# Performance work log

Hardware: AMD Instinct MI355X
Metric: run time of the kernel (lower is better)

The kernel has to match this reference:

```python
import jax, jax.numpy as jnp
import numpy as np

B, S, D, H = 2, 2048, 1024, 16
DH = D // H  # per-head attention dim


def setup_inputs() -> dict:
    key = jax.random.key(0)
    ks = jax.random.split(key, 11)
    scale = 0.02
    return {
        "query": jax.random.normal(ks[0], (B, S, D), jnp.float32),
        "key": jax.random.normal(ks[1], (B, S, D), jnp.float32),
        "value": jax.random.normal(ks[2], (B, S, D), jnp.float32),
        # per-head QKV projection weights, stacked over heads: [H, D, DH]
        "Wq": jax.random.normal(ks[3], (H, D, DH), jnp.float32) * scale,
        "bq": jnp.zeros((H, DH), jnp.float32),
        "Wk": jax.random.normal(ks[4], (H, D, DH), jnp.float32) * scale,
        "bk": jnp.zeros((H, DH), jnp.float32),
        "Wv": jax.random.normal(ks[5], (H, D, DH), jnp.float32) * scale,
        "bv": jnp.zeros((H, DH), jnp.float32),
        # output linear: [D, D]
        "Wo": jax.random.normal(ks[6], (D, D), jnp.float32) * scale,
        "bo": jnp.zeros((D,), jnp.float32),
        "look_ahead_mask": 1,
    }


def reference(query, key, value, Wq, bq, Wk, bk, Wv, bv, Wo, bo, look_ahead_mask):
    # batched per-head projections: [B,S,D] x [H,D,E] -> [B,H,S,E]
    q = jnp.einsum("bsd,hde->bhse", query, Wq) + bq[None, :, None, :]
    k = jnp.einsum("bsd,hde->bhse", key, Wk) + bk[None, :, None, :]
    v = jnp.einsum("bsd,hde->bhse", value, Wv) + bv[None, :, None, :]
    scores = jnp.einsum("bhqe,bhke->bhqk", q, k) / jnp.sqrt(jnp.float32(DH))
    if look_ahead_mask:
        causal = jnp.tril(jnp.ones((S, S), bool))
        scores = jnp.where(causal[None, None], scores, jnp.float32(-1e9))
    probs = jax.nn.softmax(scores, axis=-1)
    ctx = jnp.einsum("bhqk,bhke->bhqe", probs, v)  # [B,H,S,DH]
    # concat heads along last dim (head order matches ModuleList order)
    concat = ctx.transpose(0, 2, 1, 3).reshape(B, S, D)
    return concat @ Wo + bo
```

## Files before the change

kernel.cpp:

```cpp
#include <hip/hip_runtime.h>


typedef short bf16x8 __attribute__((ext_vector_type(8)));
typedef float f32x4 __attribute__((ext_vector_type(4)));

__device__ __forceinline__ unsigned short f2bf(float f){
  unsigned int u = __builtin_bit_cast(unsigned int, f);
  u = (u + 0x7fffu + ((u >> 16) & 1u)) >> 16;
  return (unsigned short)u;
}

__device__ __forceinline__ void gld_lds16(const void* src, void* dst){
  __builtin_amdgcn_global_load_lds((const __attribute__((address_space(1))) unsigned int*)src,
                                   (__attribute__((address_space(3))) unsigned int*)dst,
                                   16, 0, 0);
}

__device__ __forceinline__ void stage_lds(const char* gtile, size_t growb, char* lds,
                                          int tid, int rowb_lg2, int swz, int tilebytes){
  int w = tid >> 6;
  for (int c = 0; c < tilebytes; c += 4096){
    int o = c + tid*16;
    int row = o >> rowb_lg2;
    int colb = o & ((1 << rowb_lg2) - 1);
    if (swz) colb ^= ((row & 7) << 4);
    gld_lds16(gtile + (size_t)row*growb + colb, lds + c + w*1024);
  }
}

__global__ __launch_bounds__(256) void convert3(const float* __restrict__ a,
                                                const float* __restrict__ b,
                                                const float* __restrict__ c,
                                                unsigned short* __restrict__ outa,
                                                unsigned short* __restrict__ outb,
                                                unsigned short* __restrict__ outc){
  int i = blockIdx.x*blockDim.x + threadIdx.x;
  int seg = i >> 19, il = i & 524287;
  const float* in = seg==0 ? a : (seg==1 ? b : c);
  unsigned short* out = seg==0 ? outa : (seg==1 ? outb : outc);
  const float4* p = (const float4*)in;
  float4 x = p[2*il], y = p[2*il+1];
  uint4 o;
  o.x = (unsigned int)f2bf(x.x) | ((unsigned int)f2bf(x.y) << 16);
  o.y = (unsigned int)f2bf(x.z) | ((unsigned int)f2bf(x.w) << 16);
  o.z = (unsigned int)f2bf(y.x) | ((unsigned int)f2bf(y.y) << 16);
  o.w = (unsigned int)f2bf(y.z) | ((unsigned int)f2bf(y.w) << 16);
  ((uint4*)out)[il] = o;
}

__global__ __launch_bounds__(256) void transpose_bf16(const float* __restrict__ in,
                                                      unsigned short* __restrict__ out,
                                                      int R, int C,
                                                      size_t in_mstride, size_t out_mstride){
  __shared__ unsigned short tile[64][66];
  int t = threadIdx.x;
  int r0 = blockIdx.x*64, c0 = blockIdx.y*64;
  const float* inm = in + (size_t)blockIdx.z*in_mstride;
  unsigned short* outm = out + (size_t)blockIdx.z*out_mstride;
  int j = t & 63, i0 = (t >> 6)*16;
  #pragma unroll
  for (int ii = 0; ii < 16; ii++){
    int i = i0 + ii;
    tile[i][j] = f2bf(inm[(size_t)(r0+i)*C + c0 + j]);
  }
  __syncthreads();
  #pragma unroll
  for (int ii = 0; ii < 16; ii++){
    int i = i0 + ii;
    outm[(size_t)(c0+i)*R + r0 + j] = tile[j][i];
  }
}

__global__ __launch_bounds__(256) void transpose_v(const unsigned short* __restrict__ in,
                                                   unsigned short* __restrict__ out){
  __shared__ unsigned short tile[64][66];
  int t = threadIdx.x;
  int s0 = blockIdx.x*64;
  const unsigned short* inm = in + (size_t)blockIdx.y*131072;
  unsigned short* outm = out + (size_t)blockIdx.y*131072;
  int j = t & 63, i0 = (t >> 6)*16;
  #pragma unroll
  for (int ii = 0; ii < 16; ii++){
    int i = i0 + ii;
    tile[i][j] = inm[(size_t)(s0+i)*64 + j];
  }
  __syncthreads();
  #pragma unroll
  for (int ii = 0; ii < 16; ii++){
    int i = i0 + ii;
    outm[(size_t)i*2048 + s0 + j] = tile[j][i];
  }
}

template<int EPI>
__device__ __forceinline__ void gemm_body(const unsigned short* A, const unsigned short* BT,
                                          const float* bias, void* outp, float scale,
                                          unsigned short (*lA)[128*32], unsigned short (*lB)[128*32]){
  const int K = 1024, N = 1024;
  int tid = threadIdx.x, lane = tid & 63, w = tid >> 6;
  int bn = blockIdx.x*128, bm = blockIdx.y*128;
  int wm = (w >> 1)*64, wn = (w & 1)*64;
  int lr = lane & 15;
  int lkb = (lane >> 4)*16;
  const char* Ab = (const char*)(A + (size_t)bm*K);
  const char* Bb = (const char*)(BT + (size_t)bn*K);
  size_t grow = (size_t)K*2;
  int nk = K >> 5;

  f32x4 zf = {0.f,0.f,0.f,0.f};
  f32x4 acc[4][4];
  #pragma unroll
  for (int mi = 0; mi < 4; mi++)
    #pragma unroll
    for (int ni = 0; ni < 4; ni++) acc[mi][ni] = zf;

  stage_lds(Ab, grow, (char*)lA[0], tid, 6, 0, 8192);
  stage_lds(Bb, grow, (char*)lB[0], tid, 6, 0, 8192);
  __syncthreads();
  int cur = 0;
  for (int kt = 0; kt < nk; kt++){
    if (kt + 1 < nk){
      stage_lds(Ab + (size_t)(kt+1)*64, grow, (char*)lA[cur^1], tid, 6, 0, 8192);
      stage_lds(Bb + (size_t)(kt+1)*64, grow, (char*)lB[cur^1], tid, 6, 0, 8192);
    }
    const char* pa = (const char*)lA[cur];
    const char* pb = (const char*)lB[cur];
    bf16x8 af[4], bfr[4];
    #pragma unroll
    for (int mi = 0; mi < 4; mi++)
      af[mi] = *(const bf16x8*)(pa + (wm + mi*16 + lr)*64 + lkb);
    #pragma unroll
    for (int ni = 0; ni < 4; ni++)
      bfr[ni] = *(const bf16x8*)(pb + (wn + ni*16 + lr)*64 + lkb);
    #pragma unroll
    for (int mi = 0; mi < 4; mi++)
      #pragma unroll
      for (int ni = 0; ni < 4; ni++)
        acc[mi][ni] = __builtin_amdgcn_mfma_f32_16x16x32_bf16(af[mi], bfr[ni], acc[mi][ni], 0, 0, 0);
    __syncthreads();
    cur ^= 1;
  }

  #pragma unroll
  for (int mi = 0; mi < 4; mi++)
    #pragma unroll
    for (int ni = 0; ni < 4; ni++)
      #pragma unroll
      for (int r = 0; r < 4; r++){
        int row = bm + wm + mi*16 + (lane >> 4)*4 + r;
        int col = bn + wn + ni*16 + (lane & 15);
        float v = acc[mi][ni][r] + bias[col];
        if (EPI == 0){
          v *= scale;
          unsigned short* o = (unsigned short*)outp;
          o[(size_t)((row >> 11)*16 + (col >> 6))*131072 + (size_t)(row & 2047)*64 + (col & 63)] = f2bf(v);
        } else {
          float* o = (float*)outp;
          o[(size_t)row*N + col] = v;
        }
      }
}

__global__ __launch_bounds__(256) void gemm_qkv(const unsigned short* __restrict__ Xq,
                                                const unsigned short* __restrict__ Xk,
                                                const unsigned short* __restrict__ Xv,
                                                const unsigned short* __restrict__ WqT,
                                                const unsigned short* __restrict__ WkT,
                                                const unsigned short* __restrict__ WvT,
                                                const float* __restrict__ bq,
                                                const float* __restrict__ bk,
                                                const float* __restrict__ bv,
                                                unsigned short* __restrict__ oq,
                                                unsigned short* __restrict__ ok,
                                                unsigned short* __restrict__ ov){
  __shared__ __align__(16) unsigned short lA[2][128*32];
  __shared__ __align__(16) unsigned short lB[2][128*32];
  int z = blockIdx.z;
  const unsigned short* A  = z==0 ? Xq  : (z==1 ? Xk  : Xv);
  const unsigned short* BT = z==0 ? WqT : (z==1 ? WkT : WvT);
  const float* bias        = z==0 ? bq  : (z==1 ? bk  : bv);
  unsigned short* out      = z==0 ? oq  : (z==1 ? ok  : ov);
  float scale = z==0 ? 0.125f : 1.0f;
  gemm_body<0>(A, BT, bias, out, scale, lA, lB);
}

__global__ __launch_bounds__(256) void gemm_out(const unsigned short* __restrict__ A,
                                                const unsigned short* __restrict__ BT,
                                                const float* __restrict__ bias,
                                                float* __restrict__ outp){
  __shared__ __align__(16) unsigned short lA[2][128*32];
  __shared__ __align__(16) unsigned short lB[2][128*32];
  gemm_body<1>(A, BT, bias, outp, 1.0f, lA, lB);
}

__global__ __launch_bounds__(256) void attn_fwd2(const unsigned short* __restrict__ qh,
                                                 const unsigned short* __restrict__ kh,
                                                 const unsigned short* __restrict__ vt,
                                                 unsigned short* __restrict__ cc,
                                                 const int* __restrict__ maskp){
  __shared__ __align__(16) unsigned short Ps[4][16*64];
  int tid = threadIdx.x, lane = tid & 63, w = tid >> 6;
  int lg = lane >> 4, lr = lane & 15;
  int bid = blockIdx.x;
  int bh = bid & 31;
  int qquad = 31 - (bid >> 5);
  int causal = *maskp;
  int g = qquad*4 + w;
  int wq0 = g*16;
  const char* Q  = (const char*)(qh + (size_t)bh*131072);
  const char* K  = (const char*)(kh + (size_t)bh*131072);
  const char* VT = (const char*)(vt + (size_t)bh*131072);

  bf16x8 qf[2];
  #pragma unroll
  for (int kk = 0; kk < 2; kk++)
    qf[kk] = *(const bf16x8*)(Q + (size_t)(wq0 + lr)*128 + kk*64 + lg*16);

  f32x4 zf = {0.f,0.f,0.f,0.f};
  f32x4 oa[4];
  float mr[4], lsm[4];
  #pragma unroll
  for (int ei = 0; ei < 4; ei++) oa[ei] = zf;
  #pragma unroll
  for (int r = 0; r < 4; r++){ mr[r] = -1e30f; lsm[r] = 0.f; }

  int nt = causal ? (qquad + 1) : 32;

  for (int t = 0; t < nt; t++){
    bf16x8 kf[2][4];
    #pragma unroll
    for (int kk = 0; kk < 2; kk++)
      #pragma unroll
      for (int ni = 0; ni < 4; ni++)
        kf[kk][ni] = *(const bf16x8*)(K + (size_t)(t*64 + ni*16 + lr)*128 + kk*64 + lg*16);

    f32x4 sc[4];
    #pragma unroll
    for (int ni = 0; ni < 4; ni++) sc[ni] = zf;
    #pragma unroll
    for (int kk = 0; kk < 2; kk++)
      #pragma unroll
      for (int ni = 0; ni < 4; ni++)
        sc[ni] = __builtin_amdgcn_mfma_f32_16x16x32_bf16(qf[kk], kf[kk][ni], sc[ni], 0, 0, 0);

    if (causal && (t*64 + 63 > wq0)){
      #pragma unroll
      for (int ni = 0; ni < 4; ni++)
        #pragma unroll
        for (int r = 0; r < 4; r++){
          int qrow = wq0 + lg*4 + r;
          int kvc  = t*64 + ni*16 + lr;
          if (kvc > qrow) sc[ni][r] = -1e9f;
        }
    }

    #pragma unroll
    for (int r = 0; r < 4; r++){
      float mx = fmaxf(fmaxf(sc[0][r], sc[1][r]), fmaxf(sc[2][r], sc[3][r]));
      #pragma unroll
      for (int off = 1; off < 16; off <<= 1)
        mx = fmaxf(mx, __shfl_xor(mx, off, 64));
      float mo = mr[r];
      float mn = fmaxf(mo, mx);
      mr[r] = mn;
      float alpha = __expf(mo - mn);
      float psum = 0.f;
      #pragma unroll
      for (int ni = 0; ni < 4; ni++){
        float p = __expf(sc[ni][r] - mn);
        sc[ni][r] = p;
        psum += p;
      }
      #pragma unroll
      for (int off = 1; off < 16; off <<= 1)
        psum += __shfl_xor(psum, off, 64);
      lsm[r] = lsm[r]*alpha + psum;
      #pragma unroll
      for (int ei = 0; ei < 4; ei++) oa[ei][r] *= alpha;
    }

    #pragma unroll
    for (int ni = 0; ni < 4; ni++)
      #pragma unroll
      for (int r = 0; r < 4; r++){
        int prow = lg*4 + r;
        int pcb = (ni*16 + lr)*2;
        *(unsigned short*)((char*)Ps[w] + prow*128 + (pcb ^ ((prow & 7) << 4))) = f2bf(sc[ni][r]);
      }

    #pragma unroll
    for (int kk = 0; kk < 2; kk++){
      bf16x8 pf = *(const bf16x8*)((const char*)Ps[w] + lr*128 + ((kk*64 + lg*16) ^ ((lr & 7) << 4)));
      #pragma unroll
      for (int ei = 0; ei < 4; ei++){
        bf16x8 vf = *(const bf16x8*)(VT + (size_t)(ei*16 + lr)*4096 + t*128 + kk*64 + lg*16);
        oa[ei] = __builtin_amdgcn_mfma_f32_16x16x32_bf16(pf, vf, oa[ei], 0, 0, 0);
      }
    }
  }

  int b = bh >> 4, h = bh & 15;
  #pragma unroll
  for (int r = 0; r < 4; r++){
    float inv = 1.f / lsm[r];
    int q = wq0 + lg*4 + r;
    size_t rowbase = (size_t)(b*2048 + q)*1024 + h*64;
    #pragma unroll
    for (int ei = 0; ei < 4; ei++){
      int e = ei*16 + lr;
      cc[rowbase + e] = f2bf(oa[ei][r] * inv);
    }
  }
}

extern "C" void kernel_launch(void* const* d_in, const int* in_sizes, int n_in,
                              void* d_out, int out_size, void* d_ws, size_t ws_size,
                              hipStream_t stream){
  const float* query = (const float*)d_in[0];
  const float* key_i = (const float*)d_in[1];
  const float* value = (const float*)d_in[2];
  const float* Wq = (const float*)d_in[3];
  const float* bq = (const float*)d_in[4];
  const float* Wk = (const float*)d_in[5];
  const float* bk = (const float*)d_in[6];
  const float* Wv = (const float*)d_in[7];
  const float* bv = (const float*)d_in[8];
  const float* Wo = (const float*)d_in[9];
  const float* bo = (const float*)d_in[10];
  const int* mask = (const int*)d_in[11];

  char* ws = (char*)d_ws;
  const size_t ACT = 8388608;
  unsigned short* Xq  = (unsigned short*)(ws + 0*ACT);
  unsigned short* Xk  = (unsigned short*)(ws + 1*ACT);
  unsigned short* Xv  = (unsigned short*)(ws + 2*ACT);
  unsigned short* qh  = (unsigned short*)(ws + 3*ACT);
  unsigned short* kh  = (unsigned short*)(ws + 4*ACT);
  unsigned short* vh  = (unsigned short*)(ws + 5*ACT);
  unsigned short* cc  = (unsigned short*)(ws + 6*ACT);
  unsigned short* WqT = (unsigned short*)(ws + 7*ACT);
  unsigned short* WkT = (unsigned short*)(ws + 7*ACT + 2097152);
  unsigned short* WvT = (unsigned short*)(ws + 7*ACT + 4194304);
  unsigned short* WoT = (unsigned short*)(ws + 7*ACT + 6291456);
  unsigned short* vtr = Xq;

  convert3<<<6144, 256, 0, stream>>>(query, key_i, value, Xq, Xk, Xv);

  transpose_bf16<<<dim3(16,1,16), 256, 0, stream>>>(Wq, WqT, 1024, 64, 65536, 65536);
  transpose_bf16<<<dim3(16,1,16), 256, 0, stream>>>(Wk, WkT, 1024, 64, 65536, 65536);
  transpose_bf16<<<dim3(16,1,16), 256, 0, stream>>>(Wv, WvT, 1024, 64, 65536, 65536);
  transpose_bf16<<<dim3(16,16,1), 256, 0, stream>>>(Wo, WoT, 1024, 1024, 0, 0);

  gemm_qkv<<<dim3(8,32,3), 256, 0, stream>>>(Xq, Xk, Xv, WqT, WkT, WvT, bq, bk, bv, qh, kh, vh);

  transpose_v<<<dim3(32,32), 256, 0, stream>>>(vh, vtr);

  attn_fwd2<<<1024, 256, 0, stream>>>(qh, kh, vtr, cc, mask);

  gemm_out<<<dim3(8,32), 256, 0, stream>>>(cc, WoT, bo, (float*)d_out);
}
```

Baseline: 336.7 us.

## Pair low and high causal query tiles per block sharing K/V loads

Each attention block now handles two query tiles, p and 31-p, so every block does the same amount of causal work, and it launches half as many blocks. The K and V fragments loaded for each KV tile feed both query tiles, and the next K tile is prefetched into registers. A launch-bounds occupancy hint is added. The cost is higher register pressure from two sets of accumulators and prefetch buffers, and fewer blocks in flight.

```diff
diff --git a/kernel.cpp b/kernel.cpp
--- a/kernel.cpp
+++ b/kernel.cpp
@@ -193,122 +193,171 @@
   gemm_body<1>(A, BT, bias, outp, 1.0f, lA, lB);
 }
 
-__global__ __launch_bounds__(256) void attn_fwd2(const unsigned short* __restrict__ qh,
-                                                 const unsigned short* __restrict__ kh,
-                                                 const unsigned short* __restrict__ vt,
-                                                 unsigned short* __restrict__ cc,
-                                                 const int* __restrict__ maskp){
+__device__ __forceinline__ void online_sm(f32x4* sc, float* mr, float* ls, f32x4* oa){
+  #pragma unroll
+  for (int r = 0; r < 4; r++){
+    float mx = fmaxf(fmaxf(sc[0][r], sc[1][r]), fmaxf(sc[2][r], sc[3][r]));
+    #pragma unroll
+    for (int off = 1; off < 16; off <<= 1)
+      mx = fmaxf(mx, __shfl_xor(mx, off, 64));
+    float mo = mr[r];
+    float mn = fmaxf(mo, mx);
+    mr[r] = mn;
+    float alpha = __expf(mo - mn);
+    float ps = 0.f;
+    #pragma unroll
+    for (int ni = 0; ni < 4; ni++){
+      float pp = __expf(sc[ni][r] - mn);
+      sc[ni][r] = pp;
+      ps += pp;
+    }
+    #pragma unroll
+    for (int off = 1; off < 16; off <<= 1)
+      ps += __shfl_xor(ps, off, 64);
+    ls[r] = ls[r]*alpha + ps;
+    #pragma unroll
+    for (int ei = 0; ei < 4; ei++) oa[ei][r] *= alpha;
+  }
+}
+
+__device__ __forceinline__ void pv_accum(const f32x4* sc, const bf16x8 (*vf)[4], f32x4* oa,
+                                         char* Pw, int lg, int lr){
+  #pragma unroll
+  for (int ni = 0; ni < 4; ni++)
+    #pragma unroll
+    for (int r = 0; r < 4; r++){
+      int prow = lg*4 + r;
+      int pcb = (ni*16 + lr)*2;
+      *(unsigned short*)(Pw + prow*128 + (pcb ^ ((prow & 7) << 4))) = f2bf(sc[ni][r]);
+    }
+  #pragma unroll
+  for (int kk = 0; kk < 2; kk++){
+    bf16x8 pf = *(const bf16x8*)(Pw + lr*128 + ((kk*64 + lg*16) ^ ((lr & 7) << 4)));
+    #pragma unroll
+    for (int ei = 0; ei < 4; ei++)
+      oa[ei] = __builtin_amdgcn_mfma_f32_16x16x32_bf16(pf, vf[kk][ei], oa[ei], 0, 0, 0);
+  }
+}
+
+__global__ __launch_bounds__(256, 2) void attn_fwd3(const unsigned short* __restrict__ qh,
+                                                    const unsigned short* __restrict__ kh,
+                                                    const unsigned short* __restrict__ vt,
+                                                    unsigned short* __restrict__ cc,
+                                                    const int* __restrict__ maskp){
   __shared__ __align__(16) unsigned short Ps[4][16*64];
   int tid = threadIdx.x, lane = tid & 63, w = tid >> 6;
   int lg = lane >> 4, lr = lane & 15;
   int bid = blockIdx.x;
   int bh = bid & 31;
-  int qquad = 31 - (bid >> 5);
+  int p  = bid >> 5;
   int causal = *maskp;
-  int g = qquad*4 + w;
-  int wq0 = g*16;
+  int qtL = p, qtH = 31 - p;
+  int wq0L = qtL*64 + w*16, wq0H = qtH*64 + w*16;
   const char* Q  = (const char*)(qh + (size_t)bh*131072);
   const char* K  = (const char*)(kh + (size_t)bh*131072);
   const char* VT = (const char*)(vt + (size_t)bh*131072);
-
-  bf16x8 qf[2];
+  char* Pw = (char*)Ps[w];
+
+  bf16x8 qfL[2], qfH[2];
+  #pragma unroll
+  for (int kk = 0; kk < 2; kk++){
+    qfL[kk] = *(const bf16x8*)(Q + (size_t)(wq0L + lr)*128 + kk*64 + lg*16);
+    qfH[kk] = *(const bf16x8*)(Q + (size_t)(wq0H + lr)*128 + kk*64 + lg*16);
+  }
+
+  f32x4 zf = {0.f,0.f,0.f,0.f};
+  f32x4 oaL[4], oaH[4];
+  float mrL[4], lsL[4], mrH[4], lsH[4];
+  #pragma unroll
+  for (int ei = 0; ei < 4; ei++){ oaL[ei] = zf; oaH[ei] = zf; }
+  #pragma unroll
+  for (int r = 0; r < 4; r++){ mrL[r] = -1e30f; lsL[r] = 0.f; mrH[r] = -1e30f; lsH[r] = 0.f; }
+
+  int ntL = causal ? qtL + 1 : 32;
+  int ntH = causal ? qtH + 1 : 32;
+
+  bf16x8 kc[2][4], kn[2][4], vf[2][4];
   #pragma unroll
   for (int kk = 0; kk < 2; kk++)
-    qf[kk] = *(const bf16x8*)(Q + (size_t)(wq0 + lr)*128 + kk*64 + lg*16);
-
-  f32x4 zf = {0.f,0.f,0.f,0.f};
-  f32x4 oa[4];
-  float mr[4], lsm[4];
-  #pragma unroll
-  for (int ei = 0; ei < 4; ei++) oa[ei] = zf;
-  #pragma unroll
-  for (int r = 0; r < 4; r++){ mr[r] = -1e30f; lsm[r] = 0.f; }
-
-  int nt = causal ? (qquad + 1) : 32;
-
-  for (int t = 0; t < nt; t++){
-    bf16x8 kf[2][4];
+    #pragma unroll
+    for (int ni = 0; ni < 4; ni++)
+      kc[kk][ni] = *(const bf16x8*)(K + (size_t)(ni*16 + lr)*128 + kk*64 + lg*16);
+
+  for (int t = 0; t < ntH; t++){
     #pragma unroll
     for (int kk = 0; kk < 2; kk++)
       #pragma unroll
-      for (int ni = 0; ni < 4; ni++)
-        kf[kk][ni] = *(const bf16x8*)(K + (size_t)(t*64 + ni*16 + lr)*128 + kk*64 + lg*16);
-
-    f32x4 sc[4];
-    #pragma unroll
-    for (int ni = 0; ni < 4; ni++) sc[ni] = zf;
+      for (int ei = 0; ei < 4; ei++)
+        vf[kk][ei] = *(const bf16x8*)(VT + (size_t)(ei*16 + lr)*4096 + t*128 + kk*64 + lg*16);
+    if (t + 1 < ntH){
+      #pragma unroll
+      for (int kk = 0; kk < 2; kk++)
+        #pragma unroll
+        for (int ni = 0; ni < 4; ni++)
+          kn[kk][ni] = *(const bf16x8*)(K + (size_t)((t+1)*64 + ni*16 + lr)*128 + kk*64 + lg*16);
+    }
+
+    bool doL = t < ntL;
+    f32x4 scL[4], scH[4];
+    #pragma unroll
+    for (int ni = 0; ni < 4; ni++){ scL[ni] = zf; scH[ni] = zf; }
+
     #pragma unroll
     for (int kk = 0; kk < 2; kk++)
       #pragma unroll
-      for (int ni = 0; ni < 4; ni++)
-        sc[ni] = __builtin_amdgcn_mfma_f32_16x16x32_bf16(qf[kk], kf[kk][ni], sc[ni], 0, 0, 0);
-
-    if (causal && (t*64 + 63 > wq0)){
+      for (int ni = 0; ni < 4; ni++){
+        if (doL) scL[ni] = __builtin_amdgcn_mfma_f32_16x16x32_bf16(qfL[kk], kc[kk][ni], scL[ni], 0, 0, 0);
+        scH[ni] = __builtin_amdgcn_mfma_f32_16x16x32_bf16(qfH[kk], kc[kk][ni], scH[ni], 0, 0, 0);
+      }
+
+    if (causal && doL && t == qtL){
       #pragma unroll
       for (int ni = 0; ni < 4; ni++)
         #pragma unroll
         for (int r = 0; r < 4; r++){
-          int qrow = wq0 + lg*4 + r;
+          int qrow = wq0L + lg*4 + r;
           int kvc  = t*64 + ni*16 + lr;
-          if (kvc > qrow) sc[ni][r] = -1e9f;
+          if (kvc > qrow) scL[ni][r] = -1e9f;
         }
     }
-
-    #pragma unroll
-    for (int r = 0; r < 4; r++){
-      float mx = fmaxf(fmaxf(sc[0][r], sc[1][r]), fmaxf(sc[2][r], sc[3][r]));
-      #pragma unroll
-      for (int off = 1; off < 16; off <<= 1)
-        mx = fmaxf(mx, __shfl_xor(mx, off, 64));
-      float mo = mr[r];
-      float mn = fmaxf(mo, mx);
-      mr[r] = mn;
-      float alpha = __expf(mo - mn);
-      float psum = 0.f;
-      #pragma unroll
-      for (int ni = 0; ni < 4; ni++){
-        float p = __expf(sc[ni][r] - mn);
-        sc[ni][r] = p;
-        psum += p;
-      }
-      #pragma unroll
-      for (int off = 1; off < 16; off <<= 1)
-        psum += __shfl_xor(psum, off, 64);
-      lsm[r] = lsm[r]*alpha + psum;
-      #pragma unroll
-      for (int ei = 0; ei < 4; ei++) oa[ei][r] *= alpha;
-    }
-
-    #pragma unroll
-    for (int ni = 0; ni < 4; ni++)
-      #pragma unroll
-      for (int r = 0; r < 4; r++){
-        int prow = lg*4 + r;
-        int pcb = (ni*16 + lr)*2;
-        *(unsigned short*)((char*)Ps[w] + prow*128 + (pcb ^ ((prow & 7) << 4))) = f2bf(sc[ni][r]);
-      }
-
-    #pragma unroll
-    for (int kk = 0; kk < 2; kk++){
-      bf16x8 pf = *(const bf16x8*)((const char*)Ps[w] + lr*128 + ((kk*64 + lg*16) ^ ((lr & 7) << 4)));
-      #pragma unroll
-      for (int ei = 0; ei < 4; ei++){
-        bf16x8 vf = *(const bf16x8*)(VT + (size_t)(ei*16 + lr)*4096 + t*128 + kk*64 + lg*16);
-        oa[ei] = __builtin_amdgcn_mfma_f32_16x16x32_bf16(pf, vf, oa[ei], 0, 0, 0);
-      }
-    }
+    if (causal && t == qtH){
+      #pragma unroll
+      for (int ni = 0; ni < 4; ni++)
+        #pragma unroll
+        for (int r = 0; r < 4; r++){
+          int qrow = wq0H + lg*4 + r;
+          int kvc  = t*64 + ni*16 + lr;
+          if (kvc > qrow) scH[ni][r] = -1e9f;
+        }
+    }
+
+    if (doL) online_sm(scL, mrL, lsL, oaL);
+    online_sm(scH, mrH, lsH, oaH);
+
+    if (doL) pv_accum(scL, vf, oaL, Pw, lg, lr);
+    pv_accum(scH, vf, oaH, Pw, lg, lr);
+
+    #pragma unroll
+    for (int kk = 0; kk < 2; kk++)
+      #pragma unroll
+      for (int ni = 0; ni < 4; ni++)
+        kc[kk][ni] = kn[kk][ni];
   }
 
   int b = bh >> 4, h = bh & 15;
   #pragma unroll
   for (int r = 0; r < 4; r++){
-    float inv = 1.f / lsm[r];
-    int q = wq0 + lg*4 + r;
-    size_t rowbase = (size_t)(b*2048 + q)*1024 + h*64;
+    float invL = 1.f / lsL[r];
+    float invH = 1.f / lsH[r];
+    int qL = wq0L + lg*4 + r;
+    int qH = wq0H + lg*4 + r;
+    size_t rbL = (size_t)(b*2048 + qL)*1024 + h*64;
+    size_t rbH = (size_t)(b*2048 + qH)*1024 + h*64;
     #pragma unroll
     for (int ei = 0; ei < 4; ei++){
       int e = ei*16 + lr;
-      cc[rowbase + e] = f2bf(oa[ei][r] * inv);
+      cc[rbL + e] = f2bf(oaL[ei][r] * invL);
+      cc[rbH + e] = f2bf(oaH[ei][r] * invH);
     }
   }
 }
@@ -355,7 +404,7 @@
 
   transpose_v<<<dim3(32,32), 256, 0, stream>>>(vh, vtr);
 
-  attn_fwd2<<<1024, 256, 0, stream>>>(qh, kh, vtr, cc, mask);
+  attn_fwd3<<<512, 256, 0, stream>>>(qh, kh, vtr, cc, mask);
 
   gemm_out<<<dim3(8,32), 256, 0, stream>>>(cc, WoT, bo, (float*)d_out);
 }
```

After: 305.5 us. 9.3% less time.
